# Kernel tuning notes

Hardware: AMD Instinct MI355X
Metric: run time of the kernel (lower is better)

The kernel has to match this reference:

```python
import jax, jax.numpy as jnp
import numpy as np

B = 64      # batch
N = 2048    # map obstacle points
S = 4       # num_step (distinct planner per step)
A = 8       # num_anchor_per_step
H = 256     # size_middle
L = 2       # lstm num_layers
LOC = 3     # len_info_loc (x, y, theta)
WH = 64     # map_width_half == map_height_half
INTERVAL = 0.2
CIN, COUT, K, STRIDE, PAD = 4, 8, 5, 2, 2
O = (2 * WH + 2 * PAD - K) // STRIDE + 1  # 64
DLM = (2.0, 2.0, 0.5)   # delta_limit_mean
DLV = 0.1               # delta_limit_var


def setup_inputs() -> dict:
    key = jax.random.key(0)
    ks = jax.random.split(key, 16)

    def w(k, shape, fan_in):
        return jax.random.normal(k, shape, jnp.float32) / np.sqrt(fan_in)

    return {
        "inp_start_point": jax.random.normal(ks[0], (B, 1, LOC), jnp.float32),
        "map_pts": jax.random.uniform(ks[1], (2, N), jnp.float32, -12.8, 12.8),
        "ela_w1": w(ks[2], (S, H, LOC), LOC),
        "ela_w2": w(ks[3], (S, H, H), H),
        "conv_w": w(ks[4], (S, COUT, CIN, K, K), CIN * K * K),
        "elm_w1": w(ks[5], (S, H, O * O), O * O),
        "elm_w2": w(ks[6], (S, H, H), H),
        "ebl_w1": w(ks[7], (S, H, 2 * H), 2 * H),
        "ebl_w2": w(ks[8], (S, H, H), H),
        "lstm_wih": w(ks[9], (S, L, 4 * H, H), H),
        "lstm_whh": w(ks[10], (S, L, 4 * H, H), H),
        "dm_w1": w(ks[11], (S, H, H), H),
        "dm_w2": w(ks[12], (S, LOC, H), H),
        "dv_w1": w(ks[13], (S, H, H), H),
        "dv_w2": w(ks[14], (S, LOC, H), H),
    }


def _ogm(map_pts, anchor):
    """points2ogm + cal_map_last: rotate/translate global map into ego frame,
    nearest-bin argmin, scatter 1s into a [B, 128, 128] occupancy grid."""
    rel = map_pts.T[None, :, :] - anchor[:, :, 0:2]        # [B,N,2]
    m = jnp.swapaxes(rel, 1, 2)                            # [B,2,N]
    th = anchor[:, 0, 2]                                   # [B]
    c, s = jnp.cos(th), jnp.sin(th)
    rot = jnp.stack([jnp.stack([c, s], -1), jnp.stack([-s, c], -1)], axis=1)  # [B,2,2]
    pts = rot @ m                                          # [B,2,N]
    x, y = pts[:, 0], pts[:, 1]                            # [B,N]
    lim = WH * INTERVAL
    out = (jnp.abs(x) > lim) | (jnp.abs(y) > lim)
    x = jnp.where(out, 0.0, x)
    y = jnp.where(out, 0.0, y)
    centers = (jnp.arange(-WH, WH, dtype=jnp.float32) + 0.5) * INTERVAL  # [2*WH]
    x_id = jnp.argmin(jnp.abs(centers[None, None, :] - x[:, :, None]), axis=2)  # [B,N]
    y_id = jnp.argmin(jnp.abs(centers[None, None, :] - y[:, :, None]), axis=2)  # [B,N]
    b_idx = jnp.arange(B)[:, None]
    return jnp.zeros((B, 2 * WH, 2 * WH), jnp.float32).at[b_idx, x_id, y_id].set(1.0)


def _conv(x, w):
    return jax.lax.conv_general_dilated(
        x, w, (STRIDE, STRIDE), [(PAD, PAD), (PAD, PAD)],
        dimension_numbers=("NCHW", "OIHW", "NCHW"))


def _ln(x):  # LayerNorm, no affine, eps=1e-5
    mu = jnp.mean(x, axis=-1, keepdims=True)
    v = jnp.var(x, axis=-1, keepdims=True)
    return (x - mu) / jnp.sqrt(v + 1e-5)


def _mlp2(x, w1, w2):  # Linear -> ReLU -> Linear, no bias
    return jax.nn.relu(x @ w1.T) @ w2.T


def reference(inp_start_point, map_pts, ela_w1, ela_w2, conv_w, elm_w1, elm_w2,
              ebl_w1, ebl_w2, lstm_wih, lstm_whh, dm_w1, dm_w2, dv_w1, dv_w2):
    dlm = jnp.array(DLM, jnp.float32)
    anchor = inp_start_point                       # [B,1,3]
    var_last = jnp.ones_like(anchor) * 0.01
    pre_mean, pre_var = [], []
    for st in range(S):
        dm_list, dv_list = [anchor], [var_last]
        h = jnp.ones((L, B, H), jnp.float32)
        c = jnp.ones((L, B, H), jnp.float32)
        for _ in range(A - 1):
            ela = _mlp2(anchor, ela_w1[st], ela_w2[st])                 # [B,1,H]
            ogm = jax.lax.stop_gradient(_ogm(map_pts, anchor))          # [B,128,128]
            xin = jnp.broadcast_to(ogm[:, None], (B, CIN, 2 * WH, 2 * WH))
            conv = jnp.tanh(_conv(xin, conv_w[st])).sum(axis=1)         # [B,O,O]
            elm = _mlp2(conv.reshape(B, 1, O * O), elm_w1[st], elm_w2[st])  # [B,1,H]
            ebl = _mlp2(jnp.concatenate([ela, elm], axis=2), ebl_w1[st], ebl_w2[st])  # [B,1,H]
            # single-timestep multi-layer LSTM, no bias, gate order i,f,g,o
            x = ebl[:, 0]                                               # [B,H]
            for l in range(L):
                g = x @ lstm_wih[st, l].T + h[l] @ lstm_whh[st, l].T    # [B,4H]
                gi, gf, gg, go = jnp.split(g, 4, axis=-1)
                cl = jax.nn.sigmoid(gf) * c[l] + jax.nn.sigmoid(gi) * jnp.tanh(gg)
                hl = jax.nn.sigmoid(go) * jnp.tanh(cl)
                h = h.at[l].set(hl)
                c = c.at[l].set(cl)
                x = hl
            mn = _ln(x[:, None]) + ebl                                  # [B,1,H]
            r = jax.nn.relu(mn)
            anchors_now = jnp.tanh(_mlp2(r, dm_w1[st], dm_w2[st])) * dlm + anchor
            var_now = jax.nn.sigmoid(_mlp2(r, dv_w1[st], dv_w2[st])) * DLV
            anchor, var_last = anchors_now, var_now
            dm_list.append(anchors_now)
            dv_list.append(var_now)
        pre_mean.append(jnp.concatenate(dm_list, axis=1))               # [B,A,3]
        pre_var.append(jnp.concatenate(dv_list, axis=1))
    pre_mean = jnp.stack(pre_mean, axis=1)                              # [B,S,A,3]
    pre_var = jnp.stack(pre_var, axis=1)
    return pre_mean, pre_var
```

## Files before the change

### kernel.cpp

```cpp
#include <hip/hip_runtime.h>

#define WGSZ 1024
#define NWG  64

namespace {
constexpr int kN = 2048, kH = 256, kGW = 512;
constexpr size_t OFF_ELA2 = 0;
constexpr size_t OFF_ELM1 = 262144;
constexpr size_t OFF_ELM2 = 4456448;
constexpr size_t OFF_EBL1 = 4718592;
constexpr size_t OFF_EBL2 = 5242880;
constexpr size_t OFF_DM1  = 5505024;
constexpr size_t OFF_DV1  = 5767168;
constexpr size_t OFF_WIH  = 6029312;
constexpr size_t OFF_WHH  = 8126464;
constexpr size_t WS_FLOATS = 10223616;
}

__device__ __forceinline__ int bin_idx(float v) {
  float t = fmaf(v, 5.0f, 63.5f);
  int i0 = (int)floorf(t);
  int c0 = i0 - 1; c0 = c0 < 0 ? 0 : (c0 > 127 ? 127 : c0);
  int c1 = i0;     c1 = c1 < 0 ? 0 : (c1 > 127 ? 127 : c1);
  int c2 = i0 + 1; c2 = c2 < 0 ? 0 : (c2 > 127 ? 127 : c2);
  float d0 = fabsf(__fmul_rn(__fadd_rn((float)(c0 - 64), 0.5f), 0.2f) - v);
  float d1 = fabsf(__fmul_rn(__fadd_rn((float)(c1 - 64), 0.5f), 0.2f) - v);
  float d2 = fabsf(__fmul_rn(__fadd_rn((float)(c2 - 64), 0.5f), 0.2f) - v);
  int best = c0; float bd = d0;
  if (d1 < bd) { bd = d1; best = c1; }
  if (d2 < bd) { bd = d2; best = c2; }
  return best;
}

__device__ __forceinline__ float np_pw128(const float* a) {
  float r0=a[0],r1=a[1],r2=a[2],r3=a[3],r4=a[4],r5=a[5],r6=a[6],r7=a[7];
  for (int i = 8; i < 128; i += 8) {
    r0=__fadd_rn(r0,a[i+0]); r1=__fadd_rn(r1,a[i+1]);
    r2=__fadd_rn(r2,a[i+2]); r3=__fadd_rn(r3,a[i+3]);
    r4=__fadd_rn(r4,a[i+4]); r5=__fadd_rn(r5,a[i+5]);
    r6=__fadd_rn(r6,a[i+6]); r7=__fadd_rn(r7,a[i+7]);
  }
  return __fadd_rn(__fadd_rn(__fadd_rn(r0,r1),__fadd_rn(r2,r3)),
                   __fadd_rn(__fadd_rn(r4,r5),__fadd_rn(r6,r7)));
}
__device__ __forceinline__ float np_sum256(const float* a) {
  return __fadd_rn(np_pw128(a), np_pw128(a + 128));
}

__device__ __forceinline__ float sig_np(float x) {
  return __fdiv_rn(1.0f, __fadd_rn(1.0f, expf(-x)));
}

__device__ __forceinline__ void fma4(float& aa, float4 w, float4 v) {
  aa = fmaf(w.x, v.x, aa); aa = fmaf(w.y, v.y, aa);
  aa = fmaf(w.z, v.z, aa); aa = fmaf(w.w, v.w, aa);
}

__device__ __forceinline__ void gl_lds(const float4* g, float4* l) {
  __builtin_amdgcn_global_load_lds(
      (__attribute__((address_space(1))) void*)g,
      (__attribute__((address_space(3))) void*)l, 16, 0, 0);
}

template<int RA>
__device__ __forceinline__ void stage_chunk(float4* dst, const float4* wgT,
                                            const float4* wgO, int k4o,
                                            size_t Rg, int c0, int ck,
                                            int wid, int lane) {
  constexpr int RA64 = RA / 64;
  const int U = ck * RA64;
  if (wgT) {
    for (int u = wid; u < U; u += 16) {
      const int k4l = u / RA64, rg = u % RA64;
      gl_lds(wgT + (size_t)(c0 + k4l) * Rg + rg * 64 + lane, dst + u * 64);
    }
  } else {
    for (int u = wid; u < U; u += 16) {
      const int k4l = u / RA64, rg = u % RA64;
      gl_lds(wgO + (size_t)(rg * 64 + lane) * k4o + c0 + k4l, dst + u * 64);
    }
  }
}

template<int RA>
__device__ float run_matvec(float4 (*wb)[3072], const float4* wgT,
                            const float4* wgO, int k4o, size_t Rg, int K4,
                            const float4* x4, int tid, float acc0) {
  constexpr int CK4 = 3072 / RA;
  const int wid = tid >> 6, lane = tid & 63;
  float acc = acc0;
  int c0 = 0, ck = (K4 < CK4 ? K4 : CK4), cur = 0;
  stage_chunk<RA>(wb[0], wgT, wgO, k4o, Rg, 0, ck, wid, lane);
  asm volatile("s_waitcnt vmcnt(0)" ::: "memory");
  __syncthreads();
  for (;;) {
    const int nc0 = c0 + ck;
    int nck = K4 - nc0; if (nck > CK4) nck = CK4;
    if (nck > 0)
      stage_chunk<RA>(wb[cur ^ 1], wgT, wgO, k4o, Rg, nc0, nck, wid, lane);
    if (tid < RA) {
      const float4* sb = wb[cur];
      for (int kk = 0; kk < ck; ++kk)
        fma4(acc, sb[kk * RA + tid], x4[c0 + kk]);
    }
    asm volatile("s_waitcnt vmcnt(0)" ::: "memory");
    __syncthreads();
    if (nck <= 0) break;
    c0 = nc0; ck = nck; cur ^= 1;
  }
  return acc;
}

struct TransArgs {
  const float* src[9];
  float*       dst[9];
  int          n4[9];
  int          rmask[9];
  int          rshift[9];
  int          K[9];
};

__global__ void transpose_all(TransArgs a) {
  const int gtid = blockIdx.x * blockDim.x + threadIdx.x;
  const int gsz  = gridDim.x * blockDim.x;
  for (int m = 0; m < 9; ++m) {
    const float* __restrict__ src = a.src[m];
    float4* __restrict__ dst = (float4*)a.dst[m];
    const int n = a.n4[m], rm = a.rmask[m], rs = a.rshift[m], K = a.K[m];
    for (int i = gtid; i < n; i += gsz) {
      const int r = i & rm, k4 = i >> rs;
      const float* s = src + (size_t)r * K + (size_t)k4 * 4;
      float4 v; v.x = s[0]; v.y = s[1]; v.z = s[2]; v.w = s[3];
      dst[i] = v;
    }
  }
}

template<int USET>
__global__ __launch_bounds__(WGSZ, 4) void planner_kernel(
    const float* __restrict__ inp_start, const float* __restrict__ map_pts,
    const float* __restrict__ ela_w1, const float* __restrict__ ela_w2,
    const float* __restrict__ conv_w, const float* __restrict__ elm_w1,
    const float* __restrict__ elm_w2, const float* __restrict__ ebl_w1,
    const float* __restrict__ ebl_w2, const float* __restrict__ lstm_wih,
    const float* __restrict__ lstm_whh, const float* __restrict__ dm_w1,
    const float* __restrict__ dm_w2, const float* __restrict__ dv_w1,
    const float* __restrict__ dv_w2, const float* __restrict__ wsT,
    float* __restrict__ g_out) {
  const int b   = blockIdx.x;
  const int tid = threadIdx.x;
  const float4* wsf4 = (const float4*)wsT;

  __shared__ __align__(16) float4 s_wbuf[2][3072];
  __shared__ unsigned s_mask[kGW];
  __shared__ __align__(16) float s_conv[4096];
  __shared__ __align__(16) float s_cw[800];
  __shared__ __align__(16) float s_cat[512];
  __shared__ __align__(16) float s_elah[kH], s_elmh[kH], s_eblh[kH], s_eblo[kH];
  __shared__ __align__(16) float s_h0[kH], s_c0[kH], s_h1[kH], s_c1[kH];
  __shared__ __align__(16) float s_gate[1024];
  __shared__ __align__(16) float s_tmp[512];
  __shared__ __align__(16) float s_r[kH], s_dmh[kH], s_dvh[kH];
  __shared__ __align__(16) float s_ones[kH];
  __shared__ __align__(16) float s_hw[1536];
  __shared__ float s_anchor[3], s_cs[2], s_g6[6];
  __shared__ float s_mu, s_den;

  if (tid == 0) {
    float a2 = inp_start[b * 3 + 2];
    s_anchor[0] = inp_start[b * 3 + 0];
    s_anchor[1] = inp_start[b * 3 + 1];
    s_anchor[2] = a2;
    s_cs[0] = (float)cos((double)a2);
    s_cs[1] = (float)sin((double)a2);
  }
  if (tid < kH) s_ones[tid] = 1.0f;
  if (tid < 3) {
    g_out[b * 96 + tid] = inp_start[b * 3 + tid];
    g_out[6144 + b * 96 + tid] = 0.01f;
  }
  __syncthreads();

  for (int k = 0; k < 28; ++k) {
    const int st = k / 7, a = k % 7;
    const bool a0f = (a == 0);

    if (tid < kGW) s_mask[tid] = 0u;
    if (tid < 800) s_cw[tid] = conv_w[st * 800 + tid];
    if (tid >= 768 && tid < 768 + kH) {
      const int r = tid - 768;
      const float* w1r = ela_w1 + (st * kH + r) * 3;
      float h = fmaf(s_anchor[2], w1r[2],
                fmaf(s_anchor[1], w1r[1], __fmul_rn(s_anchor[0], w1r[0])));
      s_elah[r] = fmaxf(h, 0.0f);
    }
    __syncthreads();

    {
      float ax = s_anchor[0], ay = s_anchor[1], cc = s_cs[0], ss = s_cs[1];
      for (int n = tid; n < kN; n += WGSZ) {
        float mx = __fadd_rn(map_pts[n],      -ax);
        float my = __fadd_rn(map_pts[kN + n], -ay);
        float px = fmaf(ss, my, __fmul_rn(cc, mx));
        float py = fmaf(cc, my, -__fmul_rn(ss, mx));
        bool outb = (fabsf(px) > 12.8f) || (fabsf(py) > 12.8f);
        px = outb ? 0.0f : px;
        py = outb ? 0.0f : py;
        int xi = bin_idx(px), yi = bin_idx(py);
        atomicOr(&s_mask[xi * 4 + (yi >> 5)], 1u << (yi & 31));
      }
    }
    __syncthreads();

    for (int q = 0; q < 4; ++q) {
      const int p = tid + (q << 10);
      const int oy = p >> 6, ox = p & 63;
      unsigned occ = 0u;
      for (int ky = 0; ky < 5; ++ky) {
        const int y = 2 * oy - 2 + ky;
        if ((unsigned)y >= 128u) continue;
        const unsigned* row = &s_mask[y * 4];
        for (int kx = 0; kx < 5; ++kx) {
          const int x = 2 * ox - 2 + kx;
          if ((unsigned)x >= 128u) continue;
          if ((row[x >> 5] >> (x & 31)) & 1u) occ |= 1u << (ky * 5 + kx);
        }
      }
      float csum = 0.0f;
      if (occ != 0u) {
        for (int o = 0; o < 8; ++o) {
          float acc = 0.0f;
          const float* wo = s_cw + o * 100;
          for (int ci = 0; ci < 4; ++ci) {
            const float* wc = wo + ci * 25;
            #pragma unroll
            for (int t = 0; t < 25; ++t)
              acc = __fadd_rn(acc, ((occ >> t) & 1u) ? wc[t] : 0.0f);
          }
          float th = tanhf(acc);
          csum = (o == 0) ? th : __fadd_rn(csum, th);
        }
      }
      s_conv[p] = csum;
    }
    __syncthreads();

    {
      const float4* wT = USET ? wsf4 + OFF_ELA2 / 4 + st * 256 : nullptr;
      const float4* wO = USET ? nullptr
                              : (const float4*)ela_w2 + (size_t)(st * 256) * 64;
      float acc = run_matvec<256>(s_wbuf, wT, wO, 64, 1024, 64,
                                  (const float4*)s_elah, tid, 0.0f);
      if (tid < kH) s_cat[tid] = acc;
    }

    {
      const float4* wT = USET ? wsf4 + OFF_ELM1 / 4 + st * 256 : nullptr;
      const float4* wO = USET ? nullptr
                              : (const float4*)elm_w1 + (size_t)(st * 256) * 1024;
      float acc = run_matvec<256>(s_wbuf, wT, wO, 1024, 1024, 1024,
                                  (const float4*)s_conv, tid, 0.0f);
      if (tid < kH) s_elmh[tid] = fmaxf(acc, 0.0f);
    }

    {
      const float4* wT = USET ? wsf4 + OFF_ELM2 / 4 + st * 256 : nullptr;
      const float4* wO = USET ? nullptr
                              : (const float4*)elm_w2 + (size_t)(st * 256) * 64;
      float acc = run_matvec<256>(s_wbuf, wT, wO, 64, 1024, 64,
                                  (const float4*)s_elmh, tid, 0.0f);
      if (tid < kH) s_cat[256 + tid] = acc;
    }

    {
      const float4* wT = USET ? wsf4 + OFF_EBL1 / 4 + st * 256 : nullptr;
      const float4* wO = USET ? nullptr
                              : (const float4*)ebl_w1 + (size_t)(st * 256) * 128;
      float acc = run_matvec<256>(s_wbuf, wT, wO, 128, 1024, 128,
                                  (const float4*)s_cat, tid, 0.0f);
      if (tid < kH) s_eblh[tid] = fmaxf(acc, 0.0f);
    }

    {
      const float4* wT = USET ? wsf4 + OFF_EBL2 / 4 + st * 256 : nullptr;
      const float4* wO = USET ? nullptr
                              : (const float4*)ebl_w2 + (size_t)(st * 256) * 64;
      float acc = run_matvec<256>(s_wbuf, wT, wO, 64, 1024, 64,
                                  (const float4*)s_eblh, tid, 0.0f);
      if (tid < kH) s_eblo[tid] = acc;
    }

    for (int l = 0; l < 2; ++l) {
      const int rowbase = (st * 2 + l) * 1024;
      const float* xe = (l == 0) ? s_eblo : s_h0;
      const float* xh = a0f ? s_ones : ((l == 0) ? s_h0 : s_h1);
      float accA, accB;
      {
        const float4* wT = USET ? wsf4 + OFF_WIH / 4 + rowbase : nullptr;
        const float4* wO = USET ? nullptr
                                : (const float4*)lstm_wih + (size_t)rowbase * 64;
        accA = run_matvec<1024>(s_wbuf, wT, wO, 64, 8192, 64,
                                (const float4*)xe, tid, 0.0f);
      }
      {
        const float4* wT = USET ? wsf4 + OFF_WHH / 4 + rowbase : nullptr;
        const float4* wO = USET ? nullptr
                                : (const float4*)lstm_whh + (size_t)rowbase * 64;
        accB = run_matvec<1024>(s_wbuf, wT, wO, 64, 8192, 64,
                                (const float4*)xh, tid, 0.0f);
      }
      s_gate[tid] = __fadd_rn(accA, accB);
      __syncthreads();
      if (tid < kH) {
        float gi = s_gate[tid], gf = s_gate[256 + tid];
        float gg = s_gate[512 + tid], go = s_gate[768 + tid];
        float* sc = (l == 0) ? s_c0 : s_c1;
        float* sh = (l == 0) ? s_h0 : s_h1;
        float cprev = a0f ? 1.0f : sc[tid];
        float cl = __fadd_rn(__fmul_rn(sig_np(gf), cprev),
                             __fmul_rn(sig_np(gi), tanhf(gg)));
        float hl = __fmul_rn(sig_np(go), tanhf(cl));
        sc[tid] = cl; sh[tid] = hl;
      }
      __syncthreads();
    }

    if (tid < 1536)
      s_hw[tid] = (tid < 768) ? dm_w2[st * 768 + tid]
                              : dv_w2[st * 768 + tid - 768];
    if (tid == 0) s_mu = __fdiv_rn(np_sum256(s_h1), 256.0f);
    __syncthreads();
    if (tid < kH) {
      float d = __fadd_rn(s_h1[tid], -s_mu);
      s_tmp[tid] = d;
      s_tmp[256 + tid] = __fmul_rn(d, d);
    }
    __syncthreads();
    if (tid == 0) {
      float v = __fdiv_rn(np_sum256(s_tmp + 256), 256.0f);
      s_den = __fsqrt_rn(__fadd_rn(v, 1e-5f));
    }
    __syncthreads();
    if (tid < kH) {
      float r = __fadd_rn(__fdiv_rn(s_tmp[tid], s_den), s_eblo[tid]);
      s_r[tid] = fmaxf(r, 0.0f);
    }
    __syncthreads();

    {
      const float4* wT = USET ? wsf4 + OFF_DM1 / 4 + st * 256 : nullptr;
      const float4* wO = USET ? nullptr
                              : (const float4*)dm_w1 + (size_t)(st * 256) * 64;
      float acc = run_matvec<256>(s_wbuf, wT, wO, 64, 1024, 64,
                                  (const float4*)s_r, tid, 0.0f);
      if (tid < kH) s_dmh[tid] = fmaxf(acc, 0.0f);
    }
    {
      const float4* wT = USET ? wsf4 + OFF_DV1 / 4 + st * 256 : nullptr;
      const float4* wO = USET ? nullptr
                              : (const float4*)dv_w1 + (size_t)(st * 256) * 64;
      float acc = run_matvec<256>(s_wbuf, wT, wO, 64, 1024, 64,
                                  (const float4*)s_r, tid, 0.0f);
      if (tid < kH) s_dvh[tid] = fmaxf(acc, 0.0f);
    }
    __syncthreads();

    if (tid < 6) {
      const int d = tid % 3; const bool isv = tid >= 3;
      const float4* w4 = (const float4*)(s_hw + (isv ? 768 : 0) + d * 256);
      const float4* xx = (const float4*)(isv ? s_dvh : s_dmh);
      float acc = 0.0f;
      for (int i = 0; i < 64; ++i) fma4(acc, w4[i], xx[i]);
      s_g6[tid] = acc;
    }
    __syncthreads();

    if (tid == 0) {
      const float dlmf[3] = {2.0f, 2.0f, 0.5f};
      for (int d = 0; d < 3; ++d) {
        float avn = __fadd_rn(s_anchor[d], __fmul_rn(tanhf(s_g6[d]), dlmf[d]));
        float vvn = __fmul_rn(sig_np(s_g6[3 + d]), 0.1f);
        s_anchor[d] = avn;
        int o = ((b * 4 + st) * 8 + (a + 1)) * 3 + d;
        g_out[o] = avn;
        g_out[6144 + o] = vvn;
        if (a == 6 && st < 3) {
          int o2 = ((b * 4 + st + 1) * 8 + 0) * 3 + d;
          g_out[o2] = avn;
          g_out[6144 + o2] = vvn;
        }
      }
      s_cs[0] = (float)cos((double)s_anchor[2]);
      s_cs[1] = (float)sin((double)s_anchor[2]);
    }
    __syncthreads();
  }
}

extern "C" void kernel_launch(void* const* d_in, const int* in_sizes, int n_in,
                              void* d_out, int out_size, void* d_ws, size_t ws_size,
                              hipStream_t stream) {
  (void)in_sizes; (void)n_in; (void)out_size;
  const int useT = (d_ws != nullptr && ws_size >= WS_FLOATS * sizeof(float)) ? 1 : 0;
  float* wsf = (float*)d_ws;

  if (useT) {
    TransArgs ta;
    const float* srcs[9] = {
        (const float*)d_in[3],  (const float*)d_in[5],  (const float*)d_in[6],
        (const float*)d_in[7],  (const float*)d_in[8],  (const float*)d_in[11],
        (const float*)d_in[13], (const float*)d_in[9],  (const float*)d_in[10]};
    float* dsts[9] = {
        wsf + OFF_ELA2, wsf + OFF_ELM1, wsf + OFF_ELM2, wsf + OFF_EBL1,
        wsf + OFF_EBL2, wsf + OFF_DM1,  wsf + OFF_DV1,  wsf + OFF_WIH,
        wsf + OFF_WHH};
    const int n4s[9] = {65536, 1048576, 65536, 131072, 65536, 65536, 65536,
                        524288, 524288};
    const int rms[9] = {1023, 1023, 1023, 1023, 1023, 1023, 1023, 8191, 8191};
    const int rss[9] = {10, 10, 10, 10, 10, 10, 10, 13, 13};
    const int Ks[9]  = {256, 4096, 256, 512, 256, 256, 256, 256, 256};
    for (int m = 0; m < 9; ++m) {
      ta.src[m] = srcs[m]; ta.dst[m] = dsts[m]; ta.n4[m] = n4s[m];
      ta.rmask[m] = rms[m]; ta.rshift[m] = rss[m]; ta.K[m] = Ks[m];
    }
    transpose_all<<<dim3(1024), dim3(256), 0, stream>>>(ta);

    planner_kernel<1><<<dim3(NWG), dim3(WGSZ), 0, stream>>>(
        (const float*)d_in[0],  (const float*)d_in[1],  (const float*)d_in[2],
        (const float*)d_in[3],  (const float*)d_in[4],  (const float*)d_in[5],
        (const float*)d_in[6],  (const float*)d_in[7],  (const float*)d_in[8],
        (const float*)d_in[9],  (const float*)d_in[10], (const float*)d_in[11],
        (const float*)d_in[12], (const float*)d_in[13], (const float*)d_in[14],
        (const float*)wsf, (float*)d_out);
  } else {
    planner_kernel<0><<<dim3(NWG), dim3(WGSZ), 0, stream>>>(
        (const float*)d_in[0],  (const float*)d_in[1],  (const float*)d_in[2],
        (const float*)d_in[3],  (const float*)d_in[4],  (const float*)d_in[5],
        (const float*)d_in[6],  (const float*)d_in[7],  (const float*)d_in[8],
        (const float*)d_in[9],  (const float*)d_in[10], (const float*)d_in[11],
        (const float*)d_in[12], (const float*)d_in[13], (const float*)d_in[14],
        (const float*)wsf, (float*)d_out);
  }
}
```

Baseline: 9.333 ms.

## Triple-buffer matvec weight staging with fixed-size chunks and vmcnt-based waits

Replaces the double-buffered LDS weight staging (3072-float4 chunks) with a three-stage ring of 2048-float4 chunks, keeping two chunks in flight while computing on the third. Waits use partial vmcnt counts and raw s_barrier instead of draining all loads with __syncthreads each step. Each wave now issues exactly two async loads per chunk, so chunk counts are assumed to divide K4 evenly. The USET template becomes a runtime flag, which merges two kernel instantiations into one but adds a runtime branch on the load path.

```diff
diff --git a/kernel.cpp b/kernel.cpp
--- a/kernel.cpp
+++ b/kernel.cpp
@@ -65,49 +65,66 @@
 template<int RA>
 __device__ __forceinline__ void stage_chunk(float4* dst, const float4* wgT,
                                             const float4* wgO, int k4o,
-                                            size_t Rg, int c0, int ck,
+                                            int Rg, int c0,
                                             int wid, int lane) {
   constexpr int RA64 = RA / 64;
-  const int U = ck * RA64;
+  const int u0 = wid, u1 = wid + 16;
+  const int k0 = u0 / RA64, r0 = u0 % RA64;
+  const int k1 = u1 / RA64, r1 = u1 % RA64;
   if (wgT) {
-    for (int u = wid; u < U; u += 16) {
-      const int k4l = u / RA64, rg = u % RA64;
-      gl_lds(wgT + (size_t)(c0 + k4l) * Rg + rg * 64 + lane, dst + u * 64);
-    }
+    gl_lds(wgT + (size_t)(c0 + k0) * Rg + r0 * 64 + lane, dst + u0 * 64);
+    gl_lds(wgT + (size_t)(c0 + k1) * Rg + r1 * 64 + lane, dst + u1 * 64);
   } else {
-    for (int u = wid; u < U; u += 16) {
-      const int k4l = u / RA64, rg = u % RA64;
-      gl_lds(wgO + (size_t)(rg * 64 + lane) * k4o + c0 + k4l, dst + u * 64);
-    }
-  }
-}
+    gl_lds(wgO + (size_t)(r0 * 64 + lane) * k4o + c0 + k0, dst + u0 * 64);
+    gl_lds(wgO + (size_t)(r1 * 64 + lane) * k4o + c0 + k1, dst + u1 * 64);
+  }
+}
+
+#define MV_COMPUTE(BUF, CIDX)                                        \
+  do {                                                               \
+    if (tid < RA) {                                                  \
+      const float4* sb = wb[BUF];                                    \
+      const int cc0 = (CIDX) * CK4;                                  \
+      for (int kk = 0; kk < CK4; ++kk)                               \
+        fma4(acc, sb[kk * RA + tid], x4[cc0 + kk]);                  \
+    }                                                                \
+  } while (0)
 
 template<int RA>
-__device__ float run_matvec(float4 (*wb)[3072], const float4* wgT,
-                            const float4* wgO, int k4o, size_t Rg, int K4,
+__device__ float run_matvec(float4 (*wb)[2048], const float4* wgT,
+                            const float4* wgO, int k4o, int Rg, int K4,
                             const float4* x4, int tid, float acc0) {
-  constexpr int CK4 = 3072 / RA;
+  constexpr int CK4 = 2048 / RA;
   const int wid = tid >> 6, lane = tid & 63;
+  const int C = K4 / CK4;
   float acc = acc0;
-  int c0 = 0, ck = (K4 < CK4 ? K4 : CK4), cur = 0;
-  stage_chunk<RA>(wb[0], wgT, wgO, k4o, Rg, 0, ck, wid, lane);
-  asm volatile("s_waitcnt vmcnt(0)" ::: "memory");
-  __syncthreads();
-  for (;;) {
-    const int nc0 = c0 + ck;
-    int nck = K4 - nc0; if (nck > CK4) nck = CK4;
-    if (nck > 0)
-      stage_chunk<RA>(wb[cur ^ 1], wgT, wgO, k4o, Rg, nc0, nck, wid, lane);
-    if (tid < RA) {
-      const float4* sb = wb[cur];
-      for (int kk = 0; kk < ck; ++kk)
-        fma4(acc, sb[kk * RA + tid], x4[c0 + kk]);
-    }
-    asm volatile("s_waitcnt vmcnt(0)" ::: "memory");
-    __syncthreads();
-    if (nck <= 0) break;
-    c0 = nc0; ck = nck; cur ^= 1;
-  }
+  stage_chunk<RA>(wb[0], wgT, wgO, k4o, Rg, 0, wid, lane);
+  if (C > 1) stage_chunk<RA>(wb[1], wgT, wgO, k4o, Rg, CK4, wid, lane);
+  int sbuf = 2, cbuf = 0, c = 0;
+  for (; c + 2 < C; ++c) {
+    stage_chunk<RA>(wb[sbuf], wgT, wgO, k4o, Rg, (c + 2) * CK4, wid, lane);
+    asm volatile("s_waitcnt vmcnt(4) lgkmcnt(0)" ::: "memory");
+    __builtin_amdgcn_s_barrier();
+    MV_COMPUTE(cbuf, c);
+    asm volatile("s_waitcnt lgkmcnt(0)" ::: "memory");
+    __builtin_amdgcn_s_barrier();
+    sbuf = (sbuf == 2) ? 0 : sbuf + 1;
+    cbuf = (cbuf == 2) ? 0 : cbuf + 1;
+  }
+  if (c + 1 < C) {
+    asm volatile("s_waitcnt vmcnt(2) lgkmcnt(0)" ::: "memory");
+    __builtin_amdgcn_s_barrier();
+    MV_COMPUTE(cbuf, c);
+    asm volatile("s_waitcnt lgkmcnt(0)" ::: "memory");
+    __builtin_amdgcn_s_barrier();
+    cbuf = (cbuf == 2) ? 0 : cbuf + 1;
+    ++c;
+  }
+  asm volatile("s_waitcnt vmcnt(0) lgkmcnt(0)" ::: "memory");
+  __builtin_amdgcn_s_barrier();
+  MV_COMPUTE(cbuf, c);
+  asm volatile("s_waitcnt lgkmcnt(0)" ::: "memory");
+  __builtin_amdgcn_s_barrier();
   return acc;
 }
 
@@ -136,7 +153,6 @@
   }
 }
 
-template<int USET>
 __global__ __launch_bounds__(WGSZ, 4) void planner_kernel(
     const float* __restrict__ inp_start, const float* __restrict__ map_pts,
     const float* __restrict__ ela_w1, const float* __restrict__ ela_w2,
@@ -146,12 +162,12 @@
     const float* __restrict__ lstm_whh, const float* __restrict__ dm_w1,
     const float* __restrict__ dm_w2, const float* __restrict__ dv_w1,
     const float* __restrict__ dv_w2, const float* __restrict__ wsT,
-    float* __restrict__ g_out) {
+    int useT, float* __restrict__ g_out) {
   const int b   = blockIdx.x;
   const int tid = threadIdx.x;
   const float4* wsf4 = (const float4*)wsT;
 
-  __shared__ __align__(16) float4 s_wbuf[2][3072];
+  __shared__ __align__(16) float4 s_wbuf[3][2048];
   __shared__ unsigned s_mask[kGW];
   __shared__ __align__(16) float s_conv[4096];
   __shared__ __align__(16) float s_cw[800];
@@ -246,8 +262,8 @@
     __syncthreads();
 
     {
-      const float4* wT = USET ? wsf4 + OFF_ELA2 / 4 + st * 256 : nullptr;
-      const float4* wO = USET ? nullptr
+      const float4* wT = useT ? wsf4 + OFF_ELA2 / 4 + st * 256 : nullptr;
+      const float4* wO = useT ? nullptr
                               : (const float4*)ela_w2 + (size_t)(st * 256) * 64;
       float acc = run_matvec<256>(s_wbuf, wT, wO, 64, 1024, 64,
                                   (const float4*)s_elah, tid, 0.0f);
@@ -255,8 +271,8 @@
     }
 
     {
-      const float4* wT = USET ? wsf4 + OFF_ELM1 / 4 + st * 256 : nullptr;
-      const float4* wO = USET ? nullptr
+      const float4* wT = useT ? wsf4 + OFF_ELM1 / 4 + st * 256 : nullptr;
+      const float4* wO = useT ? nullptr
                               : (const float4*)elm_w1 + (size_t)(st * 256) * 1024;
       float acc = run_matvec<256>(s_wbuf, wT, wO, 1024, 1024, 1024,
                                   (const float4*)s_conv, tid, 0.0f);
@@ -264,8 +280,8 @@
     }
 
     {
-      const float4* wT = USET ? wsf4 + OFF_ELM2 / 4 + st * 256 : nullptr;
-      const float4* wO = USET ? nullptr
+      const float4* wT = useT ? wsf4 + OFF_ELM2 / 4 + st * 256 : nullptr;
+      const float4* wO = useT ? nullptr
                               : (const float4*)elm_w2 + (size_t)(st * 256) * 64;
       float acc = run_matvec<256>(s_wbuf, wT, wO, 64, 1024, 64,
                                   (const float4*)s_elmh, tid, 0.0f);
@@ -273,8 +289,8 @@
     }
 
     {
-      const float4* wT = USET ? wsf4 + OFF_EBL1 / 4 + st * 256 : nullptr;
-      const float4* wO = USET ? nullptr
+      const float4* wT = useT ? wsf4 + OFF_EBL1 / 4 + st * 256 : nullptr;
+      const float4* wO = useT ? nullptr
                               : (const float4*)ebl_w1 + (size_t)(st * 256) * 128;
       float acc = run_matvec<256>(s_wbuf, wT, wO, 128, 1024, 128,
                                   (const float4*)s_cat, tid, 0.0f);
@@ -282,8 +298,8 @@
     }
 
     {
-      const float4* wT = USET ? wsf4 + OFF_EBL2 / 4 + st * 256 : nullptr;
-      const float4* wO = USET ? nullptr
+      const float4* wT = useT ? wsf4 + OFF_EBL2 / 4 + st * 256 : nullptr;
+      const float4* wO = useT ? nullptr
                               : (const float4*)ebl_w2 + (size_t)(st * 256) * 64;
       float acc = run_matvec<256>(s_wbuf, wT, wO, 64, 1024, 64,
                                   (const float4*)s_eblh, tid, 0.0f);
@@ -296,15 +312,15 @@
       const float* xh = a0f ? s_ones : ((l == 0) ? s_h0 : s_h1);
       float accA, accB;
       {
-        const float4* wT = USET ? wsf4 + OFF_WIH / 4 + rowbase : nullptr;
-        const float4* wO = USET ? nullptr
+        const float4* wT = useT ? wsf4 + OFF_WIH / 4 + rowbase : nullptr;
+        const float4* wO = useT ? nullptr
                                 : (const float4*)lstm_wih + (size_t)rowbase * 64;
         accA = run_matvec<1024>(s_wbuf, wT, wO, 64, 8192, 64,
                                 (const float4*)xe, tid, 0.0f);
       }
       {
-        const float4* wT = USET ? wsf4 + OFF_WHH / 4 + rowbase : nullptr;
-        const float4* wO = USET ? nullptr
+        const float4* wT = useT ? wsf4 + OFF_WHH / 4 + rowbase : nullptr;
+        const float4* wO = useT ? nullptr
                                 : (const float4*)lstm_whh + (size_t)rowbase * 64;
         accB = run_matvec<1024>(s_wbuf, wT, wO, 64, 8192, 64,
                                 (const float4*)xh, tid, 0.0f);
@@ -348,16 +364,16 @@
     __syncthreads();
 
     {
-      const float4* wT = USET ? wsf4 + OFF_DM1 / 4 + st * 256 : nullptr;
-      const float4* wO = USET ? nullptr
+      const float4* wT = useT ? wsf4 + OFF_DM1 / 4 + st * 256 : nullptr;
+      const float4* wO = useT ? nullptr
                               : (const float4*)dm_w1 + (size_t)(st * 256) * 64;
       float acc = run_matvec<256>(s_wbuf, wT, wO, 64, 1024, 64,
                                   (const float4*)s_r, tid, 0.0f);
       if (tid < kH) s_dmh[tid] = fmaxf(acc, 0.0f);
     }
     {
-      const float4* wT = USET ? wsf4 + OFF_DV1 / 4 + st * 256 : nullptr;
-      const float4* wO = USET ? nullptr
+      const float4* wT = useT ? wsf4 + OFF_DV1 / 4 + st * 256 : nullptr;
+      const float4* wO = useT ? nullptr
                               : (const float4*)dv_w1 + (size_t)(st * 256) * 64;
       float acc = run_matvec<256>(s_wbuf, wT, wO, 64, 1024, 64,
                                   (const float4*)s_r, tid, 0.0f);
@@ -424,21 +440,13 @@
       ta.rmask[m] = rms[m]; ta.rshift[m] = rss[m]; ta.K[m] = Ks[m];
     }
     transpose_all<<<dim3(1024), dim3(256), 0, stream>>>(ta);
-
-    planner_kernel<1><<<dim3(NWG), dim3(WGSZ), 0, stream>>>(
-        (const float*)d_in[0],  (const float*)d_in[1],  (const float*)d_in[2],
-        (const float*)d_in[3],  (const float*)d_in[4],  (const float*)d_in[5],
-        (const float*)d_in[6],  (const float*)d_in[7],  (const float*)d_in[8],
-        (const float*)d_in[9],  (const float*)d_in[10], (const float*)d_in[11],
-        (const float*)d_in[12], (const float*)d_in[13], (const float*)d_in[14],
-        (const float*)wsf, (float*)d_out);
-  } else {
-    planner_kernel<0><<<dim3(NWG), dim3(WGSZ), 0, stream>>>(
-        (const float*)d_in[0],  (const float*)d_in[1],  (const float*)d_in[2],
-        (const float*)d_in[3],  (const float*)d_in[4],  (const float*)d_in[5],
-        (const float*)d_in[6],  (const float*)d_in[7],  (const float*)d_in[8],
-        (const float*)d_in[9],  (const float*)d_in[10], (const float*)d_in[11],
-        (const float*)d_in[12], (const float*)d_in[13], (const float*)d_in[14],
-        (const float*)wsf, (float*)d_out);
-  }
-}
+  }
+
+  planner_kernel<<<dim3(NWG), dim3(WGSZ), 0, stream>>>(
+      (const float*)d_in[0],  (const float*)d_in[1],  (const float*)d_in[2],
+      (const float*)d_in[3],  (const float*)d_in[4],  (const float*)d_in[5],
+      (const float*)d_in[6],  (const float*)d_in[7],  (const float*)d_in[8],
+      (const float*)d_in[9],  (const float*)d_in[10], (const float*)d_in[11],
+      (const float*)d_in[12], (const float*)d_in[13], (const float*)d_in[14],
+      (const float*)wsf, useT, (float*)d_out);
+}
```

After: 10.83 ms. +16.0%, slower.
